# Kernel optimization log

Hardware: AMD Instinct MI355X
Metric: run time of the kernel (lower is better)

The kernel has to match this reference:

```python
import jax, jax.numpy as jnp
import numpy as np

EPS = 1e-6

def setup_inputs() -> dict:
    key = jax.random.key(0)
    ks = jax.random.split(key, 8)
    B, S, E, C = 2, 2048, 1024, 256
    x = jax.random.normal(ks[0], (B, S, E), dtype=jnp.float32)
    mask = jnp.triu(jnp.ones((S, S), dtype=bool), k=1)  # True = masked (causal)
    conditioning = jax.random.normal(ks[1], (B, C), dtype=jnp.float32)
    sc = 1.0 / np.sqrt(E)
    Wq = jax.random.normal(ks[2], (E, E), dtype=jnp.float32) * sc
    Wk = jax.random.normal(ks[3], (E, E), dtype=jnp.float32) * sc
    Wv = jax.random.normal(ks[4], (E, E), dtype=jnp.float32) * sc
    Wo = jax.random.normal(ks[5], (E, E), dtype=jnp.float32) * sc
    rms_scale = jnp.ones((E,), dtype=jnp.float32)
    Wc = jax.random.normal(ks[6], (2 * E, C), dtype=jnp.float32) * 0.02
    bc = jax.random.normal(ks[7], (2 * E,), dtype=jnp.float32) * 0.02
    return {"x": x, "mask": mask, "conditioning": conditioning,
            "Wq": Wq, "Wk": Wk, "Wv": Wv, "Wo": Wo,
            "rms_scale": rms_scale, "Wc": Wc, "bc": bc}

def reference(x, mask, conditioning, Wq, Wk, Wv, Wo, rms_scale, Wc, bc):
    B, S, E = x.shape
    H = 16
    D = E // H
    scale = D ** -0.5
    # QKV projections (nn.Linear: x @ W.T), reshape to (B,H,S,D)
    def proj(W):
        return (x @ W.T).reshape(B, S, H, D).transpose(0, 2, 1, 3)
    q, k, v = proj(Wq), proj(Wk), proj(Wv)
    # attention scores (B,H,S,S)
    scores = jnp.einsum('bhsd,bhtd->bhst', q, k) * scale
    scores = jnp.where(mask[None, None, :, :], -jnp.inf, scores)
    attn = jax.nn.softmax(scores, axis=-1)
    out = jnp.einsum('bhst,bhtd->bhsd', attn, v)  # (B,H,S,D)
    out = out.transpose(0, 2, 1, 3).reshape(B, S, E)
    out = out @ Wo.T
    # AdaptiveRMSNorm + FiLM
    rms = jnp.sqrt(jnp.mean(out * out, axis=-1, keepdims=True) + EPS)
    xn = out / rms * rms_scale
    mod = jax.nn.silu(conditioning) @ Wc.T + bc  # (B, 2E)
    shift, sc = jnp.split(mod, 2, axis=-1)
    xn = xn * (1.0 + sc[:, None, :]) + shift[:, None, :]
    return xn
```

## Files before the change

### kernel.cpp

```cpp
#include <hip/hip_runtime.h>
#include <hip/hip_bf16.h>
#include <stdint.h>

typedef __bf16 bf16;
typedef __bf16 bf16x4 __attribute__((ext_vector_type(4)));
typedef __bf16 bf16x8 __attribute__((ext_vector_type(8)));
typedef float  f32x4  __attribute__((ext_vector_type(4)));

#define NB 2
#define NS 2048
#define NE 1024
#define NH 16
#define ND 64
#define NC 256

#define EXP2(x) __builtin_amdgcn_exp2f(x)

__device__ __forceinline__ void gload16(void* lds, const void* g) {
  __builtin_amdgcn_global_load_lds(
      (const __attribute__((address_space(1))) void*)g,
      (__attribute__((address_space(3))) void*)lds, 16, 0, 0);
}

template <int CTRL>
__device__ __forceinline__ float rowror_max(float x) {
  int xi = __builtin_bit_cast(int, x);
  int yi = __builtin_amdgcn_update_dpp(xi, xi, CTRL, 0xF, 0xF, false);
  return fmaxf(x, __builtin_bit_cast(float, yi));
}

__device__ __forceinline__ float rowmax16(float x) {
  x = rowror_max<0x121>(x);
  x = rowror_max<0x122>(x);
  x = rowror_max<0x124>(x);
  x = rowror_max<0x128>(x);
  return x;
}

__global__ __launch_bounds__(256) void cvt_all_kernel(
    const float* __restrict__ x,  const float* __restrict__ w0,
    const float* __restrict__ w1, const float* __restrict__ w2,
    const float* __restrict__ w3, bf16* __restrict__ xb,
    bf16* __restrict__ wb) {
  int blk = blockIdx.x;
  const float* s; bf16* d; int off;
  if (blk < 2048) {
    s = x; d = xb; off = blk * 2048;
  } else {
    int seg = (blk - 2048) >> 9, bb = (blk - 2048) & 511;
    const float* ws[4] = {w0, w1, w2, w3};
    s = ws[seg]; d = wb + seg * 1048576; off = bb * 2048;
  }
  int i = off + threadIdx.x * 8;
  float4 a = ((const float4*)(s + i))[0];
  float4 b = ((const float4*)(s + i))[1];
  bf16x8 o;
  o[0] = (bf16)a.x; o[1] = (bf16)a.y; o[2] = (bf16)a.z; o[3] = (bf16)a.w;
  o[4] = (bf16)b.x; o[5] = (bf16)b.y; o[6] = (bf16)b.z; o[7] = (bf16)b.w;
  *(bf16x8*)(d + i) = o;
}

__global__ __launch_bounds__(256) void mod_kernel(
    const float* __restrict__ cond, const float* __restrict__ Wc,
    const float* __restrict__ bc, float* __restrict__ mod) {
  __shared__ float scond[NC];
  int b  = blockIdx.x >> 3;
  int j0 = (blockIdx.x & 7) * 256;
  float c = cond[b * NC + threadIdx.x];
  scond[threadIdx.x] = c / (1.f + __expf(-c));
  __syncthreads();
  int j = j0 + threadIdx.x;
  float acc = bc[j];
  const float* wrow = Wc + (size_t)j * NC;
  for (int cc = 0; cc < NC; ++cc) acc += scond[cc] * wrow[cc];
  mod[b * 2 * NE + j] = acc;
}

template<int MODE>
__global__ __launch_bounds__(256) void gemm128(
    const bf16* __restrict__ A, const bf16* __restrict__ W0,
    const bf16* __restrict__ W1, const bf16* __restrict__ W2,
    void* __restrict__ out, int K) {
  __shared__ bf16 As[128 * 32];
  __shared__ bf16 Bs[128 * 32];
  const int t = threadIdx.x, w = t >> 6, l = t & 63;
  const int lr = l & 15, lg = l >> 4;
  const int wm = w >> 1, wn = w & 1;
  const int m0 = blockIdx.x * 128;
  const int ng = blockIdx.y * 128;

  const bf16* Bw;
  if (MODE == 0) {
    const bf16* Ws[3] = {W0, W1, W2};
    Bw = Ws[ng >> 10] + (size_t)(ng & 1023) * K;
  } else {
    Bw = W0 + (size_t)ng * K;
  }

  f32x4 acc[4][4];
#pragma unroll
  for (int i = 0; i < 4; ++i)
#pragma unroll
    for (int j = 0; j < 4; ++j) acc[i][j] = (f32x4){0.f, 0.f, 0.f, 0.f};

  const int srow = (l >> 2);
  const int scol = (l & 3) * 8;

  for (int kt = 0; kt < K; kt += 32) {
#pragma unroll
    for (int r = 0; r < 2; ++r) {
      int cc = w * 2 + r;
      int row = cc * 16 + srow;
      gload16((char*)As + cc * 1024, A  + (size_t)(m0 + row) * K + kt + scol);
      gload16((char*)Bs + cc * 1024, Bw + (size_t)row        * K + kt + scol);
    }
    __syncthreads();
    bf16x8 af[4], bfr[4];
#pragma unroll
    for (int i = 0; i < 4; ++i) {
      af[i]  = *(const bf16x8*)(As + (wm * 64 + i * 16 + lr) * 32 + lg * 8);
      bfr[i] = *(const bf16x8*)(Bs + (wn * 64 + i * 16 + lr) * 32 + lg * 8);
    }
#pragma unroll
    for (int i = 0; i < 4; ++i)
#pragma unroll
      for (int j = 0; j < 4; ++j)
        acc[i][j] = __builtin_amdgcn_mfma_f32_16x16x32_bf16(af[i], bfr[j], acc[i][j], 0, 0, 0);
    if (kt + 32 < K) __syncthreads();
  }

#pragma unroll
  for (int i = 0; i < 4; ++i) {
#pragma unroll
    for (int j = 0; j < 4; ++j) {
#pragma unroll
      for (int r = 0; r < 4; ++r) {
        int row = m0 + wm * 64 + i * 16 + lg * 4 + r;
        int col = ng + wn * 64 + j * 16 + lr;
        float v = acc[i][j][r];
        if (MODE == 1) {
          ((bf16*)out)[(size_t)row * NE + col] = (bf16)v;
        } else {
          int b = row >> 11, s = row & 2047;
          int wi = col >> 10, nc = col & 1023;
          int h = nc >> 6, d = nc & 63;
          size_t hb = (size_t)(b * NH + h) * 131072u;
          size_t idx;
          if (wi == 0) v *= 0.180336880f;
          if (wi == 2)
            idx = 8388608u + hb +
                  (size_t)((d >> 4) * 32768 + (s >> 3) * 128 + (d & 15) * 8 + (s & 7));
          else
            idx = (size_t)wi * 4194304u + hb +
                  (size_t)((s >> 4) * 1024 + (d >> 3) * 128 + (s & 15) * 8 + (d & 7));
          ((bf16*)out)[idx] = (bf16)v;
        }
      }
    }
  }
}

__global__ __launch_bounds__(256, 4) void attn_kernel(
    const bf16* __restrict__ Q, const bf16* __restrict__ Km,
    const bf16* __restrict__ Vt, bf16* __restrict__ O) {
  __shared__ float smrg[4][24][64];
  const int l = threadIdx.x & 63, w = threadIdx.x >> 6;
  const int lr = l & 15, lg = l >> 4;
  const int bid = blockIdx.x;
  const int xcd = bid & 7, slot = bid >> 3;
  const int bh = xcd * 4 + (slot >> 5);
  const int b = bh >> 4, h = bh & 15;
  const int sl = slot & 31;
  const int tp = sl * 2 + (w >> 1);
  const int hw = w & 1;

  bf16* pb = (bf16*)&smrg[w][0][0];

  const bf16* Qh = Q  + (size_t)bh * 131072u + l * 8;
  const bf16* Kh = Km + (size_t)bh * 131072u + l * 8;
  const bf16* Vh = Vt + (size_t)bh * 131072u + l * 8;

  bf16x8 ones;
#pragma unroll
  for (int i = 0; i < 8; ++i) ones[i] = (bf16)1.0f;

  for (int pass = 0; pass < 2; ++pass) {
    const int qbase = (pass ? (127 - tp) : tp) * 16;

    bf16x8 qf0 = *(const bf16x8*)(Qh + (qbase >> 4) * 1024);
    bf16x8 qf1 = *(const bf16x8*)(Qh + (qbase >> 4) * 1024 + 512);

    f32x4 o[4], osum;
#pragma unroll
    for (int dt = 0; dt < 4; ++dt) o[dt] = (f32x4){0.f, 0.f, 0.f, 0.f};
    osum = (f32x4){0.f, 0.f, 0.f, 0.f};
    float mrow[4];
    int qr[4];
#pragma unroll
    for (int r = 0; r < 4; ++r) { mrow[r] = -1e30f; qr[r] = qbase + lg * 4 + r; }

    for (int kv0 = hw * 64; kv0 < qbase + 16; kv0 += 128) {
      const bf16* kt = Kh + (kv0 >> 4) * 1024;
      const bf16* vt = Vh + (kv0 >> 3) * 128;
      bf16x8 k0[4], k1[4], v0[4], v1[4];
#pragma unroll
      for (int nt = 0; nt < 4; ++nt) {
        k0[nt] = *(const bf16x8*)(kt + nt * 1024);
        k1[nt] = *(const bf16x8*)(kt + nt * 1024 + 512);
      }
#pragma unroll
      for (int dt = 0; dt < 4; ++dt) {
        v0[dt] = *(const bf16x8*)(vt + dt * 32768);
        v1[dt] = *(const bf16x8*)(vt + dt * 32768 + 512);
      }
      f32x4 s[4];
#pragma unroll
      for (int nt = 0; nt < 4; ++nt) {
        f32x4 z = (f32x4){0.f, 0.f, 0.f, 0.f};
        z = __builtin_amdgcn_mfma_f32_16x16x32_bf16(qf0, k0[nt], z, 0, 0, 0);
        z = __builtin_amdgcn_mfma_f32_16x16x32_bf16(qf1, k1[nt], z, 0, 0, 0);
        s[nt] = z;
      }
      const bool edge = (kv0 + 63 > qbase);
      float pm[4];
#pragma unroll
      for (int r = 0; r < 4; ++r) pm[r] = -1e30f;
#pragma unroll
      for (int nt = 0; nt < 4; ++nt) {
        f32x4 v = s[nt];
#pragma unroll
        for (int r = 0; r < 4; ++r) {
          if (edge && (kv0 + nt * 16 + lr > qr[r])) v[r] = -1e30f;
          pm[r] = fmaxf(pm[r], v[r]);
        }
        s[nt] = v;
      }
#pragma unroll
      for (int r = 0; r < 4; ++r) pm[r] = rowmax16(pm[r]);
      int grow = 0;
#pragma unroll
      for (int r = 0; r < 4; ++r) grow |= (pm[r] > mrow[r] + 8.f);
      if (__any(grow)) {
        float al[4];
#pragma unroll
        for (int r = 0; r < 4; ++r) {
          float nm = fmaxf(mrow[r], pm[r]);
          al[r] = EXP2(mrow[r] - nm);
          mrow[r] = nm;
        }
#pragma unroll
        for (int dt = 0; dt < 4; ++dt)
#pragma unroll
          for (int r = 0; r < 4; ++r) o[dt][r] *= al[r];
#pragma unroll
        for (int r = 0; r < 4; ++r) osum[r] *= al[r];
      }
#pragma unroll
      for (int nt = 0; nt < 4; ++nt)
#pragma unroll
        for (int r = 0; r < 4; ++r)
          pb[(lg * 4 + r) * 72 + nt * 16 + lr] = (bf16)EXP2(s[nt][r] - mrow[r]);
      asm volatile("s_waitcnt lgkmcnt(0)" ::: "memory");
      __builtin_amdgcn_sched_barrier(0);
      bf16x8 pa0 = *(const bf16x8*)(pb + lr * 72 + lg * 8);
      bf16x8 pa1 = *(const bf16x8*)(pb + lr * 72 + 32 + lg * 8);
      osum = __builtin_amdgcn_mfma_f32_16x16x32_bf16(pa0, ones, osum, 0, 0, 0);
      osum = __builtin_amdgcn_mfma_f32_16x16x32_bf16(pa1, ones, osum, 0, 0, 0);
#pragma unroll
      for (int dt = 0; dt < 4; ++dt) {
        o[dt] = __builtin_amdgcn_mfma_f32_16x16x32_bf16(pa0, v0[dt], o[dt], 0, 0, 0);
        o[dt] = __builtin_amdgcn_mfma_f32_16x16x32_bf16(pa1, v1[dt], o[dt], 0, 0, 0);
      }
    }

    float* my = &smrg[w][0][0];
#pragma unroll
    for (int r = 0; r < 4; ++r) { my[r * 64 + l] = mrow[r]; my[(4 + r) * 64 + l] = osum[r]; }
#pragma unroll
    for (int dt = 0; dt < 4; ++dt)
#pragma unroll
      for (int r = 0; r < 4; ++r) my[(8 + dt * 4 + r) * 64 + l] = o[dt][r];
    __syncthreads();

    const float* pt = &smrg[w ^ 1][0][0];
    float sS[4], sP[4], rl[4];
#pragma unroll
    for (int r = 0; r < 4; ++r) {
      float mp = pt[r * 64 + l];
      float mm = fmaxf(mrow[r], mp);
      sS[r] = EXP2(mrow[r] - mm);
      sP[r] = EXP2(mp - mm);
      float lsum = sS[r] * osum[r] + sP[r] * pt[(4 + r) * 64 + l];
      rl[r] = 1.f / lsum;
    }
#pragma unroll
    for (int dd = 0; dd < 2; ++dd) {
      const int dt = hw * 2 + dd;
#pragma unroll
      for (int r = 0; r < 4; ++r) {
        float val = sS[r] * o[dt][r] + sP[r] * pt[(8 + dt * 4 + r) * 64 + l];
        O[((size_t)(b * NS) + qr[r]) * NE + h * ND + dt * 16 + lr] =
            (bf16)(val * rl[r]);
      }
    }
    __syncthreads();
  }
}

__global__ __launch_bounds__(256) void norm_kernel(
    const bf16* __restrict__ tmp, const float* __restrict__ rms_scale,
    const float* __restrict__ mod, float* __restrict__ out) {
  int row = blockIdx.x;
  int b = row >> 11;
  const bf16* trow = tmp + (size_t)row * NE;
  bf16x4 v = ((const bf16x4*)trow)[threadIdx.x];
  float vv[4] = {(float)v[0], (float)v[1], (float)v[2], (float)v[3]};
  float ss = vv[0]*vv[0] + vv[1]*vv[1] + vv[2]*vv[2] + vv[3]*vv[3];
#pragma unroll
  for (int mk = 1; mk < 64; mk <<= 1) ss += __shfl_xor(ss, mk, 64);
  __shared__ float sred[4];
  if ((threadIdx.x & 63) == 0) sred[threadIdx.x >> 6] = ss;
  __syncthreads();
  float tot = sred[0] + sred[1] + sred[2] + sred[3];
  float rinv = rsqrtf(tot * (1.f / NE) + 1e-6f);
  const float* modb = mod + b * 2 * NE;
#pragma unroll
  for (int j = 0; j < 4; ++j) {
    int e = threadIdx.x * 4 + j;
    float xn = vv[j] * rinv * rms_scale[e];
    xn = xn * (1.f + modb[NE + e]) + modb[e];
    out[(size_t)row * NE + e] = xn;
  }
}

extern "C" void kernel_launch(void* const* d_in, const int* in_sizes, int n_in,
                              void* d_out, int out_size, void* d_ws, size_t ws_size,
                              hipStream_t stream) {
  const float* x    = (const float*)d_in[0];
  const float* cond = (const float*)d_in[2];
  const float* Wq   = (const float*)d_in[3];
  const float* Wk   = (const float*)d_in[4];
  const float* Wv   = (const float*)d_in[5];
  const float* Wo   = (const float*)d_in[6];
  const float* rmss = (const float*)d_in[7];
  const float* Wc   = (const float*)d_in[8];
  const float* bc   = (const float*)d_in[9];
  float* out = (float*)d_out;

  char* ws = (char*)d_ws;
  const size_t MB = 1u << 20;
  bf16*  xb  = (bf16*)(ws);
  bf16*  Wqb = (bf16*)(ws + 8  * MB);
  bf16*  Wob = (bf16*)(ws + 14 * MB);
  bf16*  Qb  = (bf16*)(ws + 16 * MB);
  bf16*  Kb  = (bf16*)(ws + 24 * MB);
  bf16*  Vt  = (bf16*)(ws + 32 * MB);
  bf16*  Oa  = (bf16*)(ws);
  bf16*  tmp = (bf16*)(ws + 16 * MB);
  float* mod = (float*)(ws + 40 * MB);

  mod_kernel<<<16, 256, 0, stream>>>(cond, Wc, bc, mod);

  cvt_all_kernel<<<4096, 256, 0, stream>>>(x, Wq, Wk, Wv, Wo, xb, Wqb);

  gemm128<0><<<dim3(32, 24), 256, 0, stream>>>(xb, Wqb, Wqb + 1048576, Wqb + 2097152, Qb, NE);

  attn_kernel<<<1024, 256, 0, stream>>>(Qb, Kb, Vt, Oa);

  gemm128<1><<<dim3(32, 8), 256, 0, stream>>>(Oa, Wob, nullptr, nullptr, tmp, NE);

  norm_kernel<<<NB * NS, 256, 0, stream>>>(tmp, rmss, mod, out);
}
```

Before: 134.8 us.

## Software-pipeline PV matmul one step behind QK in attention; fuse mod into convert

The attention loop now computes the softmax probabilities for the current KV tile while doing the P·V MFMA for the previous tile. The probabilities go into a double-buffered LDS tile, and a tail step drains the last tile. The aim is to overlap the LDS write/read latency and the V loads with the QK MFMAs. The separate FiLM modulation kernel is folded into the conversion kernel as extra blocks, which saves one launch. This relies on the pb scratch having room for two buffers per wave, and the overlap adds register pressure.

```diff
diff --git a/kernel.cpp b/kernel.cpp
--- a/kernel.cpp
+++ b/kernel.cpp
@@ -41,8 +41,25 @@
     const float* __restrict__ x,  const float* __restrict__ w0,
     const float* __restrict__ w1, const float* __restrict__ w2,
     const float* __restrict__ w3, bf16* __restrict__ xb,
-    bf16* __restrict__ wb) {
+    bf16* __restrict__ wb,
+    const float* __restrict__ cond, const float* __restrict__ Wc,
+    const float* __restrict__ bc, float* __restrict__ mod) {
   int blk = blockIdx.x;
+  if (blk >= 4096) {
+    __shared__ float scond[NC];
+    int mb = blk - 4096;
+    int b  = mb >> 3;
+    int j0 = (mb & 7) * 256;
+    float c = cond[b * NC + threadIdx.x];
+    scond[threadIdx.x] = c / (1.f + __expf(-c));
+    __syncthreads();
+    int j = j0 + threadIdx.x;
+    float acc = bc[j];
+    const float* wrow = Wc + (size_t)j * NC;
+    for (int cc = 0; cc < NC; ++cc) acc += scond[cc] * wrow[cc];
+    mod[b * 2 * NE + j] = acc;
+    return;
+  }
   const float* s; bf16* d; int off;
   if (blk < 2048) {
     s = x; d = xb; off = blk * 2048;
@@ -58,22 +75,6 @@
   o[0] = (bf16)a.x; o[1] = (bf16)a.y; o[2] = (bf16)a.z; o[3] = (bf16)a.w;
   o[4] = (bf16)b.x; o[5] = (bf16)b.y; o[6] = (bf16)b.z; o[7] = (bf16)b.w;
   *(bf16x8*)(d + i) = o;
-}
-
-__global__ __launch_bounds__(256) void mod_kernel(
-    const float* __restrict__ cond, const float* __restrict__ Wc,
-    const float* __restrict__ bc, float* __restrict__ mod) {
-  __shared__ float scond[NC];
-  int b  = blockIdx.x >> 3;
-  int j0 = (blockIdx.x & 7) * 256;
-  float c = cond[b * NC + threadIdx.x];
-  scond[threadIdx.x] = c / (1.f + __expf(-c));
-  __syncthreads();
-  int j = j0 + threadIdx.x;
-  float acc = bc[j];
-  const float* wrow = Wc + (size_t)j * NC;
-  for (int cc = 0; cc < NC; ++cc) acc += scond[cc] * wrow[cc];
-  mod[b * 2 * NE + j] = acc;
 }
 
 template<int MODE>
@@ -199,19 +200,16 @@
 #pragma unroll
     for (int r = 0; r < 4; ++r) { mrow[r] = -1e30f; qr[r] = qbase + lg * 4 + r; }
 
+    int bufi = 0;
+    int prev_kv0 = -1;
+
     for (int kv0 = hw * 64; kv0 < qbase + 16; kv0 += 128) {
       const bf16* kt = Kh + (kv0 >> 4) * 1024;
-      const bf16* vt = Vh + (kv0 >> 3) * 128;
-      bf16x8 k0[4], k1[4], v0[4], v1[4];
+      bf16x8 k0[4], k1[4];
 #pragma unroll
       for (int nt = 0; nt < 4; ++nt) {
         k0[nt] = *(const bf16x8*)(kt + nt * 1024);
         k1[nt] = *(const bf16x8*)(kt + nt * 1024 + 512);
-      }
-#pragma unroll
-      for (int dt = 0; dt < 4; ++dt) {
-        v0[dt] = *(const bf16x8*)(vt + dt * 32768);
-        v1[dt] = *(const bf16x8*)(vt + dt * 32768 + 512);
       }
       f32x4 s[4];
 #pragma unroll
@@ -221,6 +219,27 @@
         z = __builtin_amdgcn_mfma_f32_16x16x32_bf16(qf1, k1[nt], z, 0, 0, 0);
         s[nt] = z;
       }
+      if (prev_kv0 >= 0) {
+        const bf16* vt = Vh + (prev_kv0 >> 3) * 128;
+        bf16x8 v0[4], v1[4];
+#pragma unroll
+        for (int dt = 0; dt < 4; ++dt) {
+          v0[dt] = *(const bf16x8*)(vt + dt * 32768);
+          v1[dt] = *(const bf16x8*)(vt + dt * 32768 + 512);
+        }
+        asm volatile("s_waitcnt lgkmcnt(0)" ::: "memory");
+        __builtin_amdgcn_sched_barrier(0);
+        const bf16* pbR = pb + (bufi ^ 1) * 1152;
+        bf16x8 pa0 = *(const bf16x8*)(pbR + lr * 72 + lg * 8);
+        bf16x8 pa1 = *(const bf16x8*)(pbR + lr * 72 + 32 + lg * 8);
+        osum = __builtin_amdgcn_mfma_f32_16x16x32_bf16(pa0, ones, osum, 0, 0, 0);
+        osum = __builtin_amdgcn_mfma_f32_16x16x32_bf16(pa1, ones, osum, 0, 0, 0);
+#pragma unroll
+        for (int dt = 0; dt < 4; ++dt) {
+          o[dt] = __builtin_amdgcn_mfma_f32_16x16x32_bf16(pa0, v0[dt], o[dt], 0, 0, 0);
+          o[dt] = __builtin_amdgcn_mfma_f32_16x16x32_bf16(pa1, v1[dt], o[dt], 0, 0, 0);
+        }
+      }
       const bool edge = (kv0 + 63 > qbase);
       float pm[4];
 #pragma unroll
@@ -255,15 +274,29 @@
 #pragma unroll
         for (int r = 0; r < 4; ++r) osum[r] *= al[r];
       }
+      bf16* pbW = pb + bufi * 1152;
 #pragma unroll
       for (int nt = 0; nt < 4; ++nt)
 #pragma unroll
         for (int r = 0; r < 4; ++r)
-          pb[(lg * 4 + r) * 72 + nt * 16 + lr] = (bf16)EXP2(s[nt][r] - mrow[r]);
+          pbW[(lg * 4 + r) * 72 + nt * 16 + lr] = (bf16)EXP2(s[nt][r] - mrow[r]);
+      prev_kv0 = kv0;
+      bufi ^= 1;
+    }
+
+    if (prev_kv0 >= 0) {
+      const bf16* vt = Vh + (prev_kv0 >> 3) * 128;
+      bf16x8 v0[4], v1[4];
+#pragma unroll
+      for (int dt = 0; dt < 4; ++dt) {
+        v0[dt] = *(const bf16x8*)(vt + dt * 32768);
+        v1[dt] = *(const bf16x8*)(vt + dt * 32768 + 512);
+      }
       asm volatile("s_waitcnt lgkmcnt(0)" ::: "memory");
       __builtin_amdgcn_sched_barrier(0);
-      bf16x8 pa0 = *(const bf16x8*)(pb + lr * 72 + lg * 8);
-      bf16x8 pa1 = *(const bf16x8*)(pb + lr * 72 + 32 + lg * 8);
+      const bf16* pbR = pb + (bufi ^ 1) * 1152;
+      bf16x8 pa0 = *(const bf16x8*)(pbR + lr * 72 + lg * 8);
+      bf16x8 pa1 = *(const bf16x8*)(pbR + lr * 72 + 32 + lg * 8);
       osum = __builtin_amdgcn_mfma_f32_16x16x32_bf16(pa0, ones, osum, 0, 0, 0);
       osum = __builtin_amdgcn_mfma_f32_16x16x32_bf16(pa1, ones, osum, 0, 0, 0);
 #pragma unroll
@@ -359,9 +392,8 @@
   bf16*  tmp = (bf16*)(ws + 16 * MB);
   float* mod = (float*)(ws + 40 * MB);
 
-  mod_kernel<<<16, 256, 0, stream>>>(cond, Wc, bc, mod);
-
-  cvt_all_kernel<<<4096, 256, 0, stream>>>(x, Wq, Wk, Wv, Wo, xb, Wqb);
+  cvt_all_kernel<<<4112, 256, 0, stream>>>(x, Wq, Wk, Wv, Wo, xb, Wqb,
+                                           cond, Wc, bc, mod);
 
   gemm128<0><<<dim3(32, 24), 256, 0, stream>>>(xb, Wqb, Wqb + 1048576, Wqb + 2097152, Qb, NE);
 
```

After: 134.2 us. Within noise of the previous version (-0.4%).
